# Kernel optimization log

Hardware: AMD Instinct MI355X
Metric: run time of the kernel (lower is better)

Reference implementation:

```python
import jax, jax.numpy as jnp
import numpy as np

ALPHA = 1.0
LAMBDA_CL = 1.0
EPS = 1e-08


def setup_inputs() -> dict:
    key = jax.random.key(0)
    k1, k2, k3, k4 = jax.random.split(key, 4)
    N, D_IN, D_LAT, K = 16384, 1024, 128, 256
    x = jax.random.normal(k1, (N, D_IN), dtype=jnp.float32)
    h_x = jax.random.normal(k2, (N, D_LAT), dtype=jnp.float32)
    a_x = jax.random.normal(k3, (N, D_IN), dtype=jnp.float32)
    cluster_centers = jax.random.normal(k4, (K, D_LAT), dtype=jnp.float32)
    return {"x": x, "h_x": h_x, "a_x": a_x, "cluster_centers": cluster_centers}


def _pairwise_dist(h, R):
    # Euclidean cdist via ||h||^2 + ||R||^2 - 2 h R^T (avoids [N,K,d] broadcast)
    h2 = jnp.sum(h * h, axis=1, keepdims=True)            # [N,1]
    r2 = jnp.sum(R * R, axis=1)[None, :]                   # [1,K]
    d2 = h2 + r2 - 2.0 * jnp.einsum('nd,kd->nk', h, R)     # [N,K]
    return jnp.sqrt(jnp.maximum(d2, 0.0))


def reference(x, h_x, a_x, cluster_centers):
    # Reconstruction MSE
    loss_reconstr = jnp.mean((x - a_x) ** 2)
    # Alpha-smoothed soft assignments (note +EPS in denominator, as in original)
    dist = _pairwise_dist(h_x, cluster_centers)            # [N,K]
    e = jnp.exp(-ALPHA * dist)                             # [N,K]
    soft_assignments = e / (jnp.sum(e, axis=1, keepdims=True) + EPS)
    # Weighted centers and clustering MSE
    weighted_centers = jnp.einsum('nk,kd->nd', soft_assignments, cluster_centers)
    loss_clustering = jnp.mean((h_x - weighted_centers) ** 2)
    return loss_reconstr + LAMBDA_CL * loss_clustering
```

## Files before the change

kernel.cpp:

```cpp
#include <hip/hip_runtime.h>
#include <math.h>

#define N_ROWS 16384
#define D_INP  1024
#define D_LAT  128
#define KC     256
#define EPS_F  1e-8f

typedef __attribute__((ext_vector_type(8))) short short8v;
typedef _Float16 half8v __attribute__((ext_vector_type(8)));
typedef __attribute__((ext_vector_type(4))) float floatx4;

__device__ __forceinline__ unsigned short f2bf(float f) {
    unsigned u = __float_as_uint(f);
    return (unsigned short)((u + 0x7FFFu + ((u >> 16) & 1u)) >> 16);
}
__device__ __forceinline__ unsigned short f2h(float f) {
    _Float16 h = (_Float16)f;
    unsigned short u;
    __builtin_memcpy(&u, &h, 2);
    return u;
}

__global__ __launch_bounds__(256) void prep_kernel(const float* __restrict__ R,
        unsigned short* __restrict__ Rf16, unsigned short* __restrict__ Rtb,
        float* __restrict__ r2) {
    const int t = threadIdx.x;
    const int kc = blockIdx.x * 2 + (t >> 7);
    const int d = t & 127;
    const float v = R[kc * D_LAT + d];
    Rf16[kc * D_LAT + d] = f2h(v);
    Rtb[d * KC + kc] = f2bf(v);
    float sq = v * v;
    for (int off = 32; off > 0; off >>= 1) sq += __shfl_down(sq, off);
    __shared__ float s4[4];
    if ((t & 63) == 0) s4[t >> 6] = sq;
    __syncthreads();
    if (t == 0)   r2[kc] = s4[0] + s4[1];
    if (t == 128) r2[kc] = s4[2] + s4[3];
}

__global__ __launch_bounds__(512) void fused_kernel(
        const float* __restrict__ x, const float* __restrict__ a,
        const float* __restrict__ h,
        const unsigned short* __restrict__ Rf16,
        const unsigned short* __restrict__ Rtb,
        const float* __restrict__ r2w,
        float* __restrict__ pr, float* __restrict__ pc) {
    __shared__ float sh32[16 * 132];
    __shared__ unsigned short sh16[16 * 136];
    __shared__ unsigned short eL[16 * 264];
    __shared__ float sumsL[16][16];
    __shared__ float h2L[16];
    __shared__ float invL[16];
    __shared__ float swL[8];

    const int bid = blockIdx.x;
    const int tid = threadIdx.x;

    if (bid & 1) {
        const int rid = bid >> 1;
        const int gid = rid * 512 + tid;
        const float4* x4 = (const float4*)x;
        const float4* a4 = (const float4*)a;
        float4 xv[8], av[8];
#pragma unroll
        for (int it = 0; it < 8; ++it) {
            const int i = gid + it * (512 * 1024);
            xv[it] = x4[i];
            av[it] = a4[i];
        }
        float a0 = 0.f, a1 = 0.f, a2 = 0.f, a3 = 0.f;
#pragma unroll
        for (int it = 0; it < 8; ++it) {
            const float d0 = xv[it].x - av[it].x, d1 = xv[it].y - av[it].y;
            const float d2 = xv[it].z - av[it].z, d3 = xv[it].w - av[it].w;
            a0 = fmaf(d0, d0, a0);
            a1 = fmaf(d1, d1, a1);
            a2 = fmaf(d2, d2, a2);
            a3 = fmaf(d3, d3, a3);
        }
        float acc = (a0 + a1) + (a2 + a3);
        for (int off = 32; off > 0; off >>= 1) acc += __shfl_down(acc, off);
        if ((tid & 63) == 0) swL[tid >> 6] = acc;
        __syncthreads();
        if (tid == 0) {
            float t = 0.f;
#pragma unroll
            for (int w = 0; w < 8; ++w) t += swL[w];
            pr[rid] = t;
        }
        return;
    }

    const int cid = bid >> 1;
    const int rbase = cid * 16;
    const int wv = tid >> 6, lane = tid & 63;
    const int g = lane >> 4, c = lane & 15;

    {
        const int r = tid >> 5, c4 = tid & 31;
        const float4 v = *(const float4*)(h + (size_t)(rbase + r) * D_LAT + c4 * 4);
        *(float4*)&sh32[r * 132 + c4 * 4] = v;
        sh16[r * 136 + c4 * 4 + 0] = f2h(v.x);
        sh16[r * 136 + c4 * 4 + 1] = f2h(v.y);
        sh16[r * 136 + c4 * 4 + 2] = f2h(v.z);
        sh16[r * 136 + c4 * 4 + 3] = f2h(v.w);
        float s = v.x * v.x + v.y * v.y + v.z * v.z + v.w * v.w;
        s += __shfl_xor(s, 1);
        s += __shfl_xor(s, 2);
        s += __shfl_xor(s, 4);
        s += __shfl_xor(s, 8);
        s += __shfl_xor(s, 16);
        if ((tid & 31) == 0) h2L[r] = s;
    }
    __syncthreads();

    half8v afr[4];
#pragma unroll
    for (int ks = 0; ks < 4; ++ks)
        afr[ks] = *(const half8v*)&sh16[c * 136 + ks * 32 + g * 8];
    float h2a[4];
#pragma unroll
    for (int i = 0; i < 4; ++i) h2a[i] = h2L[4 * g + i];

#pragma unroll
    for (int tt = 0; tt < 2; ++tt) {
        const int tile = wv * 2 + tt;
        const int kc = tile * 16 + c;
        floatx4 acc = {0.f, 0.f, 0.f, 0.f};
#pragma unroll
        for (int ks = 0; ks < 4; ++ks) {
            const half8v b = *(const half8v*)(Rf16 + (size_t)kc * D_LAT + ks * 32 + g * 8);
            acc = __builtin_amdgcn_mfma_f32_16x16x32_f16(afr[ks], b, acc, 0, 0, 0);
        }
        const float r2v = r2w[kc];
#pragma unroll
        for (int i = 0; i < 4; ++i) {
            const float d2 = h2a[i] + r2v - 2.0f * acc[i];
            const float e = __expf(-sqrtf(fmaxf(d2, 0.f)));
            eL[(4 * g + i) * 264 + kc] = f2bf(e);
            float v = e;
            v += __shfl_xor(v, 1);
            v += __shfl_xor(v, 2);
            v += __shfl_xor(v, 4);
            v += __shfl_xor(v, 8);
            if (c == 0) sumsL[4 * g + i][tile] = v;
        }
    }
    __syncthreads();
    if (tid < 16) {
        float t = 0.f;
#pragma unroll
        for (int j = 0; j < 16; ++j) t += sumsL[tid][j];
        invL[tid] = 1.0f / (t + EPS_F);
    }
    __syncthreads();

    const int dcol = wv * 16 + c;
    float inva[4];
#pragma unroll
    for (int i = 0; i < 4; ++i) inva[i] = invL[4 * g + i];
    floatx4 acc = {0.f, 0.f, 0.f, 0.f};
#pragma unroll
    for (int ks = 0; ks < 8; ++ks) {
        const short8v ae = *(const short8v*)&eL[c * 264 + ks * 32 + g * 8];
        const short8v b = *(const short8v*)(Rtb + (size_t)dcol * KC + ks * 32 + g * 8);
        acc = __builtin_amdgcn_mfma_f32_16x16x32_bf16(ae, b, acc, 0, 0, 0);
    }
    float lp = 0.f;
#pragma unroll
    for (int i = 0; i < 4; ++i) {
        const float wc = acc[i] * inva[i];
        const float hv = sh32[(4 * g + i) * 132 + dcol];
        const float df = hv - wc;
        lp = fmaf(df, df, lp);
    }
    for (int off = 32; off > 0; off >>= 1) lp += __shfl_down(lp, off);
    if (lane == 0) swL[wv] = lp;
    __syncthreads();
    if (tid == 0) {
        float t = 0.f;
#pragma unroll
        for (int w = 0; w < 8; ++w) t += swL[w];
        pc[cid] = t;
    }
}

__global__ __launch_bounds__(256) void finalize_kernel(const float* __restrict__ pr,
                                                       const float* __restrict__ pc,
                                                       float* __restrict__ out) {
    const int tid = threadIdx.x;
    float a = 0.f, b = 0.f;
    for (int i = tid; i < 1024; i += 256) a += pr[i];
    for (int i = tid; i < 1024; i += 256) b += pc[i];
    float v = a * (1.0f / ((float)N_ROWS * (float)D_INP)) +
              b * (1.0f / ((float)N_ROWS * (float)D_LAT));
    for (int off = 32; off > 0; off >>= 1) v += __shfl_down(v, off);
    __shared__ float sw[4];
    if ((tid & 63) == 0) sw[tid >> 6] = v;
    __syncthreads();
    if (tid == 0) out[0] = sw[0] + sw[1] + sw[2] + sw[3];
}

extern "C" void kernel_launch(void* const* d_in, const int* in_sizes, int n_in,
                              void* d_out, int out_size, void* d_ws, size_t ws_size,
                              hipStream_t stream) {
    const float* x = (const float*)d_in[0];
    const float* h = (const float*)d_in[1];
    const float* a = (const float*)d_in[2];
    const float* R = (const float*)d_in[3];
    float* out = (float*)d_out;
    char* wsb = (char*)d_ws;
    float* pr = (float*)(wsb + 0);
    float* pc = (float*)(wsb + 8192);
    float* r2 = (float*)(wsb + 12288);
    unsigned short* Rf16 = (unsigned short*)(wsb + 16384);
    unsigned short* Rtb  = (unsigned short*)(wsb + 16384 + 65536);

    prep_kernel<<<128, 256, 0, stream>>>(R, Rf16, Rtb, r2);
    fused_kernel<<<2048, 512, 0, stream>>>(x, a, h, Rf16, Rtb, r2, pr, pc);
    finalize_kernel<<<1, 256, 0, stream>>>(pr, pc, out);
}
```

Baseline: 46.21 us.

## Stream reconstruction loads through direct-to-LDS ring buffer with manual waitcnt

The MSE blocks now issue global_load_lds copies of x and a into a per-wave triple-buffered LDS ring, using explicit vmcnt/lgkmcnt waits, instead of loading 16 float4s into registers. Each block now reads a contiguous chunk rather than grid-strided addresses. All shared buffers are merged into a 48KB arena. This is meant to pipeline memory traffic and reduce register pressure, but the larger LDS footprint can lower occupancy for both block types.

Result: no change. 46.15 us (-0.1%).

```diff
diff --git a/kernel.cpp b/kernel.cpp
--- a/kernel.cpp
+++ b/kernel.cpp
@@ -20,6 +20,11 @@
     unsigned short u;
     __builtin_memcpy(&u, &h, 2);
     return u;
+}
+__device__ __forceinline__ void gll16(const void* g, void* l) {
+    __builtin_amdgcn_global_load_lds(
+        (const __attribute__((address_space(1))) void*)g,
+        (__attribute__((address_space(3))) void*)l, 16, 0, 0);
 }
 
 __global__ __launch_bounds__(256) void prep_kernel(const float* __restrict__ R,
@@ -47,55 +52,72 @@
         const unsigned short* __restrict__ Rtb,
         const float* __restrict__ r2w,
         float* __restrict__ pr, float* __restrict__ pc) {
-    __shared__ float sh32[16 * 132];
-    __shared__ unsigned short sh16[16 * 136];
-    __shared__ unsigned short eL[16 * 264];
-    __shared__ float sumsL[16][16];
-    __shared__ float h2L[16];
-    __shared__ float invL[16];
-    __shared__ float swL[8];
+    __shared__ __align__(16) char arena[49152];
+    __shared__ float rsw[8];
 
     const int bid = blockIdx.x;
     const int tid = threadIdx.x;
+    const int wv = tid >> 6, lane = tid & 63;
 
     if (bid & 1) {
         const int rid = bid >> 1;
-        const int gid = rid * 512 + tid;
-        const float4* x4 = (const float4*)x;
-        const float4* a4 = (const float4*)a;
-        float4 xv[8], av[8];
-#pragma unroll
-        for (int it = 0; it < 8; ++it) {
-            const int i = gid + it * (512 * 1024);
-            xv[it] = x4[i];
-            av[it] = a4[i];
-        }
+        const float4* xg = (const float4*)x + (size_t)rid * 4096 + wv * 512 + lane;
+        const float4* ag = (const float4*)a + (size_t)rid * 4096 + wv * 512 + lane;
+        char* slot = arena + wv * 6144;
         float a0 = 0.f, a1 = 0.f, a2 = 0.f, a3 = 0.f;
-#pragma unroll
-        for (int it = 0; it < 8; ++it) {
-            const float d0 = xv[it].x - av[it].x, d1 = xv[it].y - av[it].y;
-            const float d2 = xv[it].z - av[it].z, d3 = xv[it].w - av[it].w;
-            a0 = fmaf(d0, d0, a0);
-            a1 = fmaf(d1, d1, a1);
-            a2 = fmaf(d2, d2, a2);
-            a3 = fmaf(d3, d3, a3);
-        }
+
+#define ISSUE(j) do { \
+            gll16(xg + (j) * 64, slot + ((j) % 3) * 2048); \
+            gll16(ag + (j) * 64, slot + ((j) % 3) * 2048 + 1024); \
+        } while (0)
+#define WAITVM(n) asm volatile("s_waitcnt vmcnt(" #n ")" ::: "memory")
+#define LGKM0()   asm volatile("s_waitcnt lgkmcnt(0)" ::: "memory")
+#define CONSUME(j) do { \
+            const float4 xv = *(const float4*)(slot + ((j) % 3) * 2048 + lane * 16); \
+            const float4 av = *(const float4*)(slot + ((j) % 3) * 2048 + 1024 + lane * 16); \
+            const float d0 = xv.x - av.x, d1 = xv.y - av.y; \
+            const float d2 = xv.z - av.z, d3 = xv.w - av.w; \
+            a0 = fmaf(d0, d0, a0); a1 = fmaf(d1, d1, a1); \
+            a2 = fmaf(d2, d2, a2); a3 = fmaf(d3, d3, a3); \
+        } while (0)
+
+        ISSUE(0); ISSUE(1); ISSUE(2);
+        WAITVM(4); CONSUME(0); LGKM0(); ISSUE(3);
+        WAITVM(4); CONSUME(1); LGKM0(); ISSUE(4);
+        WAITVM(4); CONSUME(2); LGKM0(); ISSUE(5);
+        WAITVM(4); CONSUME(3); LGKM0(); ISSUE(6);
+        WAITVM(4); CONSUME(4); LGKM0(); ISSUE(7);
+        WAITVM(4); CONSUME(5);
+        WAITVM(2); CONSUME(6);
+        WAITVM(0); CONSUME(7);
+#undef ISSUE
+#undef WAITVM
+#undef LGKM0
+#undef CONSUME
+
         float acc = (a0 + a1) + (a2 + a3);
         for (int off = 32; off > 0; off >>= 1) acc += __shfl_down(acc, off);
-        if ((tid & 63) == 0) swL[tid >> 6] = acc;
+        if (lane == 0) rsw[wv] = acc;
         __syncthreads();
         if (tid == 0) {
             float t = 0.f;
 #pragma unroll
-            for (int w = 0; w < 8; ++w) t += swL[w];
+            for (int w = 0; w < 8; ++w) t += rsw[w];
             pr[rid] = t;
         }
         return;
     }
 
+    float* sh32          = (float*)(arena);
+    unsigned short* sh16 = (unsigned short*)(arena + 8448);
+    unsigned short* eLp  = (unsigned short*)(arena + 12800);
+    float (*sumsL)[16]   = (float(*)[16])(arena + 21248);
+    float* h2L           = (float*)(arena + 22272);
+    float* invL          = (float*)(arena + 22336);
+    float* swL           = (float*)(arena + 22400);
+
     const int cid = bid >> 1;
     const int rbase = cid * 16;
-    const int wv = tid >> 6, lane = tid & 63;
     const int g = lane >> 4, c = lane & 15;
 
     {
@@ -139,7 +161,7 @@
         for (int i = 0; i < 4; ++i) {
             const float d2 = h2a[i] + r2v - 2.0f * acc[i];
             const float e = __expf(-sqrtf(fmaxf(d2, 0.f)));
-            eL[(4 * g + i) * 264 + kc] = f2bf(e);
+            eLp[(4 * g + i) * 264 + kc] = f2bf(e);
             float v = e;
             v += __shfl_xor(v, 1);
             v += __shfl_xor(v, 2);
@@ -164,7 +186,7 @@
     floatx4 acc = {0.f, 0.f, 0.f, 0.f};
 #pragma unroll
     for (int ks = 0; ks < 8; ++ks) {
-        const short8v ae = *(const short8v*)&eL[c * 264 + ks * 32 + g * 8];
+        const short8v ae = *(const short8v*)&eLp[c * 264 + ks * 32 + g * 8];
         const short8v b = *(const short8v*)(Rtb + (size_t)dcol * KC + ks * 32 + g * 8);
         acc = __builtin_amdgcn_mfma_f32_16x16x32_bf16(ae, b, acc, 0, 0, 0);
     }
```
